# Kernel optimization log

Hardware: AMD Instinct MI355X
Metric: run time of the kernel (lower is better)

## Reference

```python
import jax, jax.numpy as jnp
import numpy as np

V, E = 100000, 128   # vocab, embed_size
B, S, N = 32, 1024, 16  # batch, seq_len, n_negatives


def setup_inputs() -> dict:
    key = jax.random.key(0)
    k1, k2, k3, k4 = jax.random.split(key, 4)
    sentence = jax.random.randint(k1, (B, S), 0, V, dtype=jnp.int64)
    context = jax.random.normal(k2, (B, S, E), dtype=jnp.float32)
    # WalkerAlias negative sampling happens on CPU in the original; here the
    # sampled indices are precomputed inputs (uniform counter ** power -> uniform).
    neg_samples = jax.random.randint(k3, (B, S, N), 0, V, dtype=jnp.int64)
    W = jax.random.normal(k4, (V, E), dtype=jnp.float32) * 0.02
    return {"sentence": sentence, "context": context, "neg_samples": neg_samples, "W": W}


def reference(sentence, context, neg_samples, W):
    emb = W[sentence]                                   # [B,S,E] gather
    pos_loss = jax.nn.log_sigmoid(jnp.sum(emb * context, axis=-1))          # [B,S]
    neg_emb = W[neg_samples]                            # [B,S,N,E] gather
    neg_scores = jnp.einsum('bsne,bse->bsn', neg_emb, context)              # [B,S,N]
    neg_loss = jnp.sum(jax.nn.log_sigmoid(-neg_scores), axis=-1)            # [B,S]
    return -jnp.sum(pos_loss + neg_loss)
```

## Files before the change

kernel.cpp:

```cpp
#include <hip/hip_runtime.h>
#include <hip/hip_bf16.h>
#include <cmath>

#define NS_ROWS    32768
#define NS_NEG     16
#define NS_TARGETS 17
#define NS_TILE    15
#define NS_CPAD    132

__device__ __forceinline__ float log_sigmoid_f(float x) {
    return fminf(x, 0.0f) - log1pf(__expf(-fabsf(x)));
}

__global__ __launch_bounds__(256) void neg_sampling_kernel(
    const int*   __restrict__ sentence,
    const float* __restrict__ context,
    const int*   __restrict__ neg,
    const float* __restrict__ W,
    float*       __restrict__ out)
{
    __shared__ float cctx[NS_TILE][NS_CPAD];

    const int tid     = threadIdx.x;
    const int rowbase = blockIdx.x * NS_TILE;

    for (int i = tid; i < NS_TILE * 32; i += 256) {
        const int r  = i >> 5;
        const int e4 = i & 31;
        const int grow = rowbase + r;
        if (grow < NS_ROWS) {
            const float4 v = reinterpret_cast<const float4*>(context)[grow * 32 + e4];
            *reinterpret_cast<float4*>(&cctx[r][e4 * 4]) = v;
        }
    }
    __syncthreads();

    float loss = 0.0f;
    if (tid < NS_TILE * NS_TARGETS) {
        const int lrow = (tid * 241) >> 12;
        const int tgt  = tid - lrow * NS_TARGETS;
        const int row  = rowbase + lrow;
        if (row < NS_ROWS) {
            const int idx = (tgt == 0) ? sentence[row]
                                       : neg[row * NS_NEG + (tgt - 1)];
            const float4* __restrict__ wr =
                reinterpret_cast<const float4*>(W) + (long)idx * 32;
            const float4* __restrict__ cr =
                reinterpret_cast<const float4*>(&cctx[lrow][0]);

            float acc = 0.0f;
#pragma unroll 8
            for (int e = 0; e < 32; ++e) {
                const float4 w = wr[e];
                const float4 c = cr[e];
                acc += w.x * c.x + w.y * c.y + w.z * c.z + w.w * c.w;
            }
            const float x = (tgt == 0) ? acc : -acc;
            loss = log_sigmoid_f(x);
        }
    }

#pragma unroll
    for (int m = 32; m >= 1; m >>= 1) loss += __shfl_xor(loss, m, 64);

    __shared__ float smem[4];
    const int wave = tid >> 6, lane = tid & 63;
    if (lane == 0) smem[wave] = loss;
    __syncthreads();
    if (tid == 0) {
        atomicAdd(out, -(smem[0] + smem[1] + smem[2] + smem[3]));
    }
}

extern "C" void kernel_launch(void* const* d_in, const int* in_sizes, int n_in,
                              void* d_out, int out_size, void* d_ws, size_t ws_size,
                              hipStream_t stream) {
    const int*   sentence = (const int*)d_in[0];
    const float* context  = (const float*)d_in[1];
    const int*   neg      = (const int*)d_in[2];
    const float* W        = (const float*)d_in[3];
    float*       out      = (float*)d_out;

    hipMemsetAsync(out, 0, sizeof(float), stream);

    const int blocks = (NS_ROWS + NS_TILE - 1) / NS_TILE;
    neg_sampling_kernel<<<blocks, 256, 0, stream>>>(sentence, context, neg, W, out);
}
```

Measured before the change: 59.23 us.

## Split each row dot product across four lanes and prefetch W before barrier

Each (row, target) dot product is now handled by a group of four threads instead of one, with blocks enlarged to 1024 threads. Each lane loads a strided quarter of the gathered W row into registers before the context tile barrier, so the random gathers overlap with the context staging. Partial sums are combined with two shuffles. The changes are meant to spread the gather latency over more in-flight loads and shorten each thread's serial loop, at the cost of larger blocks and more idle threads (255 active groups out of 256).

```diff
diff --git a/kernel.cpp b/kernel.cpp
--- a/kernel.cpp
+++ b/kernel.cpp
@@ -12,7 +12,7 @@
     return fminf(x, 0.0f) - log1pf(__expf(-fabsf(x)));
 }
 
-__global__ __launch_bounds__(256) void neg_sampling_kernel(
+__global__ __launch_bounds__(1024) void neg_sampling_kernel(
     const int*   __restrict__ sentence,
     const float* __restrict__ context,
     const int*   __restrict__ neg,
@@ -20,13 +20,32 @@
     float*       __restrict__ out)
 {
     __shared__ float cctx[NS_TILE][NS_CPAD];
+    __shared__ float wsum[16];
 
     const int tid     = threadIdx.x;
     const int rowbase = blockIdx.x * NS_TILE;
 
-    for (int i = tid; i < NS_TILE * 32; i += 256) {
-        const int r  = i >> 5;
-        const int e4 = i & 31;
+    const int group = tid >> 2;
+    const int sub   = tid & 3;
+    const int lrow  = group / NS_TARGETS;
+    const int tgt   = group - lrow * NS_TARGETS;
+    const int row   = rowbase + lrow;
+    const bool active = (lrow < NS_TILE) && (row < NS_ROWS);
+
+    float4 w0, w1, w2, w3, w4, w5, w6, w7;
+    if (active) {
+        const int idx = (tgt == 0) ? sentence[row] : neg[row * NS_NEG + (tgt - 1)];
+        const float4* __restrict__ wr =
+            reinterpret_cast<const float4*>(W) + (size_t)idx * 32 + sub;
+        w0 = wr[0];  w1 = wr[4];  w2 = wr[8];  w3 = wr[12];
+        w4 = wr[16]; w5 = wr[20]; w6 = wr[24]; w7 = wr[28];
+    } else {
+        w0=w1=w2=w3=w4=w5=w6=w7 = make_float4(0.f,0.f,0.f,0.f);
+    }
+
+    if (tid < NS_TILE * 32) {
+        const int r  = tid >> 5;
+        const int e4 = tid & 31;
         const int grow = rowbase + r;
         if (grow < NS_ROWS) {
             const float4 v = reinterpret_cast<const float4*>(context)[grow * 32 + e4];
@@ -36,39 +55,46 @@
     __syncthreads();
 
     float loss = 0.0f;
-    if (tid < NS_TILE * NS_TARGETS) {
-        const int lrow = (tid * 241) >> 12;
-        const int tgt  = tid - lrow * NS_TARGETS;
-        const int row  = rowbase + lrow;
-        if (row < NS_ROWS) {
-            const int idx = (tgt == 0) ? sentence[row]
-                                       : neg[row * NS_NEG + (tgt - 1)];
-            const float4* __restrict__ wr =
-                reinterpret_cast<const float4*>(W) + (long)idx * 32;
-            const float4* __restrict__ cr =
-                reinterpret_cast<const float4*>(&cctx[lrow][0]);
-
-            float acc = 0.0f;
-#pragma unroll 8
-            for (int e = 0; e < 32; ++e) {
-                const float4 w = wr[e];
-                const float4 c = cr[e];
-                acc += w.x * c.x + w.y * c.y + w.z * c.z + w.w * c.w;
-            }
-            const float x = (tgt == 0) ? acc : -acc;
-            loss = log_sigmoid_f(x);
+    if (active) {
+        const float* crow = &cctx[lrow][0];
+        float acc = 0.0f;
+        {
+            float4 c;
+            c = *reinterpret_cast<const float4*>(crow + (sub +  0) * 4);
+            acc += w0.x*c.x + w0.y*c.y + w0.z*c.z + w0.w*c.w;
+            c = *reinterpret_cast<const float4*>(crow + (sub +  4) * 4);
+            acc += w1.x*c.x + w1.y*c.y + w1.z*c.z + w1.w*c.w;
+            c = *reinterpret_cast<const float4*>(crow + (sub +  8) * 4);
+            acc += w2.x*c.x + w2.y*c.y + w2.z*c.z + w2.w*c.w;
+            c = *reinterpret_cast<const float4*>(crow + (sub + 12) * 4);
+            acc += w3.x*c.x + w3.y*c.y + w3.z*c.z + w3.w*c.w;
+            c = *reinterpret_cast<const float4*>(crow + (sub + 16) * 4);
+            acc += w4.x*c.x + w4.y*c.y + w4.z*c.z + w4.w*c.w;
+            c = *reinterpret_cast<const float4*>(crow + (sub + 20) * 4);
+            acc += w5.x*c.x + w5.y*c.y + w5.z*c.z + w5.w*c.w;
+            c = *reinterpret_cast<const float4*>(crow + (sub + 24) * 4);
+            acc += w6.x*c.x + w6.y*c.y + w6.z*c.z + w6.w*c.w;
+            c = *reinterpret_cast<const float4*>(crow + (sub + 28) * 4);
+            acc += w7.x*c.x + w7.y*c.y + w7.z*c.z + w7.w*c.w;
+        }
+        acc += __shfl_xor(acc, 1, 64);
+        acc += __shfl_xor(acc, 2, 64);
+        if (sub == 0) {
+            loss = log_sigmoid_f((tgt == 0) ? acc : -acc);
         }
     }
 
 #pragma unroll
     for (int m = 32; m >= 1; m >>= 1) loss += __shfl_xor(loss, m, 64);
 
-    __shared__ float smem[4];
     const int wave = tid >> 6, lane = tid & 63;
-    if (lane == 0) smem[wave] = loss;
+    if (lane == 0) wsum[wave] = loss;
     __syncthreads();
     if (tid == 0) {
-        atomicAdd(out, -(smem[0] + smem[1] + smem[2] + smem[3]));
+        float t = 0.0f;
+#pragma unroll
+        for (int i = 0; i < 16; ++i) t += wsum[i];
+        atomicAdd(out, -t);
     }
 }
 
@@ -84,5 +110,5 @@
     hipMemsetAsync(out, 0, sizeof(float), stream);
 
     const int blocks = (NS_ROWS + NS_TILE - 1) / NS_TILE;
-    neg_sampling_kernel<<<blocks, 256, 0, stream>>>(sentence, context, neg, W, out);
+    neg_sampling_kernel<<<blocks, 1024, 0, stream>>>(sentence, context, neg, W, out);
 }
```

New measurement: 51.89 us. 1.14x faster.
